# Performance work log

Measured on AMD Instinct MI355X. Metric: run time of the kernel, lower is better.

The kernel has to match this reference:

```python
import jax, jax.numpy as jnp
import numpy as np

B, T, M, D, H, DK, DV = 2, 1024, 1024, 1024, 16, 64, 64
R = 2 * T + M  # number of relative positions required by rel_shift path


def setup_inputs() -> dict:
    key = jax.random.key(0)
    ks = jax.random.split(key, 11)
    s = 0.02
    return {
        "inputs": jax.random.normal(ks[0], (B, T, D), jnp.float32),
        "attention_mask": jnp.ones((B, T, M + T), jnp.float32),
        "positional_encodings": jax.random.normal(ks[1], (R, D), jnp.float32),
        "memory": jax.random.normal(ks[2], (B, M, D), jnp.float32),
        "Wq": jax.random.normal(ks[3], (D, H * DK), jnp.float32) * s,
        "Wk": jax.random.normal(ks[4], (D, H * DK), jnp.float32) * s,
        "Wv": jax.random.normal(ks[5], (D, H * DV), jnp.float32) * s,
        "Wr": jax.random.normal(ks[6], (D, H * DK), jnp.float32) * s,
        "r_w_bias": jax.random.normal(ks[7], (H, DK), jnp.float32) * s,
        "r_r_bias": jax.random.normal(ks[8], (H, DK), jnp.float32) * s,
        "W_out": jax.random.normal(ks[9], (H * DV, D), jnp.float32) * s,
    }


def _rel_shift(m, attention_length):
    # m: [T_q, T_q + L] -> [T_q, L], TXL relative shift via reshape/slice
    tq, total = m.shape
    x = m.reshape(total, tq)[1:].reshape(tq, total - 1)
    return x[:, :attention_length]


def reference(inputs, attention_mask, positional_encodings, memory,
              Wq, Wk, Wv, Wr, r_w_bias, r_r_bias, W_out):
    b, t, d = inputs.shape
    values = jnp.concatenate([memory, inputs], axis=1)  # [B, L, D]
    L = values.shape[1]
    q = (inputs @ Wq).reshape(b, t, H, DK)
    k = (values @ Wk).reshape(b, L, H, DK)
    v = (values @ Wv).reshape(b, L, H, DV)
    rk = (positional_encodings @ Wr).reshape(-1, H, DK)  # [R, H, DK]
    # content + relative logits (TXL)
    content = jnp.einsum('bthd,bThd->bhtT', q + r_w_bias, k)        # [B,H,T,L]
    rel = jnp.einsum('bthd,rhd->bhtr', q + r_r_bias, rk)            # [B,H,T,R]
    rel = jax.vmap(jax.vmap(lambda m: _rel_shift(m, L)))(rel)       # [B,H,T,L]
    logits = (content + rel) * (DK ** -0.5)
    masked = logits - (1.0 - attention_mask[:, None, :, :]) * 1e30
    w = jax.nn.softmax(masked, axis=-1)
    attn = jnp.einsum('bhtT,bThd->bthd', w, v)                      # [B,T,H,DV]
    return attn.reshape(b, t, H * DV) @ W_out
```

## Files before the change

### kernel.cpp

```cpp
#include <hip/hip_runtime.h>
#include <hip/hip_fp16.h>
#include <stdint.h>

#define Bz 2
#define Tq 1024
#define Mm 1024
#define Hh 16
#define Ll 2048
#define Rr 3072

typedef __attribute__((ext_vector_type(8))) short bf16x8;
typedef __attribute__((ext_vector_type(4))) float f32x4;

typedef __attribute__((address_space(3))) uint8_t lds_u8_t;
typedef __attribute__((address_space(1))) uint8_t glb_u8_t;

__device__ __forceinline__ void gl2lds16(const void* g, void* l) {
  __builtin_amdgcn_global_load_lds((const glb_u8_t*)g, (lds_u8_t*)l, 16, 0, 0);
}

__device__ __forceinline__ unsigned short f2bf(float f) {
  unsigned int u = __builtin_bit_cast(unsigned int, f);
  u = u + 0x7fffu + ((u >> 16) & 1u);
  return (unsigned short)(u >> 16);
}
__device__ __forceinline__ float b2f(unsigned short s) {
  unsigned int u = ((unsigned int)s) << 16;
  return __builtin_bit_cast(float, u);
}
__device__ __forceinline__ unsigned int cvt_pk_bf16(float lo, float hi) {
  unsigned int r;
  asm volatile("v_cvt_pk_bf16_f32 %0, %1, %2" : "=v"(r) : "v"(lo), "v"(hi));
  return r;
}

__global__ __launch_bounds__(256) void k_prep2(
    const float* __restrict__ x, const float* __restrict__ mem,
    const float* __restrict__ pos,
    const float* __restrict__ w0, const float* __restrict__ w1,
    const float* __restrict__ w2, const float* __restrict__ w3,
    const float* __restrict__ w4,
    unsigned short* __restrict__ vin, unsigned short* __restrict__ pb,
    unsigned short* __restrict__ t0, unsigned short* __restrict__ t1,
    unsigned short* __restrict__ t2, unsigned short* __restrict__ t3,
    unsigned short* __restrict__ t4) {
  __shared__ float tile[64][65];
  int bid = blockIdx.x;
  if (bid < 4096) {
    int idx = bid * 256 + threadIdx.x;
    int e = idx << 2;
    int row = e >> 10, col = e & 1023;
    int b = row >> 11, l = row & 2047;
    const float* s = (l < Mm) ? (mem + (((size_t)b * Mm + l) << 10) + col)
                              : (x + (((size_t)b * Tq + (l - Mm)) << 10) + col);
    float4 v = *(const float4*)s;
    ushort4 o;
    o.x = f2bf(v.x); o.y = f2bf(v.y); o.z = f2bf(v.z); o.w = f2bf(v.w);
    *(ushort4*)(vin + e) = o;
  } else if (bid < 7168) {
    int idx = (bid - 4096) * 256 + threadIdx.x;
    int e = idx << 2;
    float4 v = *(const float4*)(pos + e);
    ushort4 t;
    t.x = f2bf(v.x); t.y = f2bf(v.y); t.z = f2bf(v.z); t.w = f2bf(v.w);
    *(ushort4*)(pb + e) = t;
  } else {
    int r3 = bid - 7168;
    int mz = r3 >> 8, rem = r3 & 255;
    const float* W;
    unsigned short* WT;
    switch (mz) {
      case 0: W = w0; WT = t0; break;
      case 1: W = w1; WT = t1; break;
      case 2: W = w2; WT = t2; break;
      case 3: W = w3; WT = t3; break;
      default: W = w4; WT = t4; break;
    }
    int k0 = (rem >> 4) * 64, n0 = (rem & 15) * 64;
    int tid = threadIdx.x;
    int rr = tid >> 4, c4 = (tid & 15) * 4;
#pragma unroll
    for (int it = 0; it < 4; ++it) {
      int r = rr + it * 16;
      float4 v = *(const float4*)(W + (size_t)(k0 + r) * 1024 + n0 + c4);
      tile[r][c4] = v.x; tile[r][c4 + 1] = v.y;
      tile[r][c4 + 2] = v.z; tile[r][c4 + 3] = v.w;
    }
    __syncthreads();
#pragma unroll
    for (int it = 0; it < 4; ++it) {
      int n = rr + it * 16;
      ushort4 o;
      o.x = f2bf(tile[c4 + 0][n]); o.y = f2bf(tile[c4 + 1][n]);
      o.z = f2bf(tile[c4 + 2][n]); o.w = f2bf(tile[c4 + 3][n]);
      *(ushort4*)(WT + (size_t)(n0 + n) * 1024 + k0 + c4) = o;
    }
  }
}

template <int RMAP>
__device__ __forceinline__ void gemm_pipe(const unsigned short* __restrict__ A,
                                          const unsigned short* __restrict__ Bt,
                                          int m0, int n0, unsigned short* As,
                                          unsigned short* Bs, f32x4 acc[4][4]) {
  const int tid = threadIdx.x;
  const int w = tid >> 6, lane = tid & 63;
  const int quad = lane >> 4, li = lane & 15;
  const int wr = w >> 1, wc = w & 1;
  f32x4 z = {0.f, 0.f, 0.f, 0.f};
#pragma unroll
  for (int mi = 0; mi < 4; ++mi)
#pragma unroll
    for (int ni = 0; ni < 4; ++ni) acc[mi][ni] = z;

  const int rs = lane >> 2;
  const int cs = lane & 3;

#pragma unroll
  for (int s = 0; s < 2; ++s) {
    int i = w * 2 + s;
    int r = i * 16 + rs;
    int c = cs ^ ((r >> 1) & 3);
    int ar = m0 + r;
    if (RMAP) ar = ar + 1024 + (ar & 1024);
    gl2lds16(A + (size_t)ar * 1024 + c * 8, (char*)As + i * 1024);
    gl2lds16(Bt + (size_t)(n0 + r) * 1024 + c * 8, (char*)Bs + i * 1024);
  }

  for (int k0 = 0; k0 < 1024; k0 += 32) {
    const int bo = ((k0 >> 5) & 1) * 8192;
    const int no = bo ^ 8192;
    __builtin_amdgcn_s_waitcnt(0x0F70);
    __syncthreads();
    if (k0 + 32 < 1024) {
#pragma unroll
      for (int s = 0; s < 2; ++s) {
        int i = w * 2 + s;
        int r = i * 16 + rs;
        int c = cs ^ ((r >> 1) & 3);
        int ar = m0 + r;
        if (RMAP) ar = ar + 1024 + (ar & 1024);
        gl2lds16(A + (size_t)ar * 1024 + k0 + 32 + c * 8,
                 (char*)As + no + i * 1024);
        gl2lds16(Bt + (size_t)(n0 + r) * 1024 + k0 + 32 + c * 8,
                 (char*)Bs + no + i * 1024);
      }
    }
    bf16x8 af[4], bfr[4];
#pragma unroll
    for (int mi = 0; mi < 4; ++mi) {
      int r = wr * 64 + mi * 16 + li;
      int ch = quad ^ ((r >> 1) & 3);
      af[mi] = *(const bf16x8*)((const char*)As + bo + r * 64 + ch * 16);
    }
#pragma unroll
    for (int ni = 0; ni < 4; ++ni) {
      int r = wc * 64 + ni * 16 + li;
      int ch = quad ^ ((r >> 1) & 3);
      bfr[ni] = *(const bf16x8*)((const char*)Bs + bo + r * 64 + ch * 16);
    }
#pragma unroll
    for (int mi = 0; mi < 4; ++mi)
#pragma unroll
      for (int ni = 0; ni < 4; ++ni)
        acc[mi][ni] = __builtin_amdgcn_mfma_f32_16x16x32_bf16(
            af[mi], bfr[ni], acc[mi][ni], 0, 0, 0);
  }
}

__global__ __launch_bounds__(256) void k_proj(
    const unsigned short* __restrict__ Vin, const unsigned short* __restrict__ Pb,
    const unsigned short* __restrict__ WqT, const unsigned short* __restrict__ WkT,
    const unsigned short* __restrict__ WvT, const unsigned short* __restrict__ WrT,
    unsigned short* __restrict__ qb, unsigned short* __restrict__ kb,
    unsigned short* __restrict__ vtb, unsigned short* __restrict__ rkb) {
  __shared__ unsigned short As[2 * 128 * 32];
  __shared__ unsigned short Bs[2 * 128 * 32];
  const int t = blockIdx.x;
  const int tid = threadIdx.x, w = tid >> 6, lane = tid & 63;
  const int quad = lane >> 4, li = lane & 15, wr = w >> 1, wc = w & 1;
  f32x4 acc[4][4];

  if (t < 256) {
    int a = t & 7, n = (t >> 3) & 7, c = t >> 6;
    int m0 = (4 * a + c) * 128, n0 = n * 128;
    gemm_pipe<0>(Vin, WkT, m0, n0, As, Bs, acc);
#pragma unroll
    for (int mi = 0; mi < 4; ++mi)
#pragma unroll
      for (int ni = 0; ni < 4; ++ni)
#pragma unroll
        for (int reg = 0; reg < 4; ++reg) {
          int rrow = m0 + wr * 64 + mi * 16 + quad * 4 + reg;
          int cc = n0 + wc * 64 + ni * 16 + li;
          kb[(size_t)rrow * 1024 + cc] = f2bf(acc[mi][ni][reg]);
        }
  } else if (t < 512) {
    int f = t - 256;
    int a = f & 7, n = (f >> 3) & 7, c = f >> 6;
    int m0 = (4 * a + c) * 128, n0 = n * 128;
    gemm_pipe<0>(Vin, WvT, m0, n0, As, Bs, acc);
#pragma unroll
    for (int mi = 0; mi < 4; ++mi)
#pragma unroll
      for (int ni = 0; ni < 4; ++ni) {
        int r0 = m0 + wr * 64 + mi * 16 + quad * 4;
        int b = r0 >> 11, l0 = r0 & 2047;
        int cc = n0 + wc * 64 + ni * 16 + li;
        ushort4 o;
        o.x = f2bf(acc[mi][ni][0]); o.y = f2bf(acc[mi][ni][1]);
        o.z = f2bf(acc[mi][ni][2]); o.w = f2bf(acc[mi][ni][3]);
        *(ushort4*)(vtb + ((size_t)(b * 1024 + cc)) * Ll + l0) = o;
      }
  } else if (t < 640) {
    int f = t - 512;
    int a = f & 7, n = (f >> 3) & 7, c = f >> 6;
    int m0 = (2 * a + c) * 128, n0 = n * 128;
    gemm_pipe<1>(Vin, WqT, m0, n0, As, Bs, acc);
#pragma unroll
    for (int mi = 0; mi < 4; ++mi)
#pragma unroll
      for (int ni = 0; ni < 4; ++ni)
#pragma unroll
        for (int reg = 0; reg < 4; ++reg) {
          int rrow = m0 + wr * 64 + mi * 16 + quad * 4 + reg;
          int cc = n0 + wc * 64 + ni * 16 + li;
          qb[(size_t)rrow * 1024 + cc] = f2bf(acc[mi][ni][reg]);
        }
  } else {
    int f = t - 640;
    int a = f & 7, n = (f >> 3) & 7, c = f >> 6;
    int m0 = (3 * a + c) * 128, n0 = n * 128;
    gemm_pipe<0>(Pb, WrT, m0, n0, As, Bs, acc);
#pragma unroll
    for (int mi = 0; mi < 4; ++mi)
#pragma unroll
      for (int ni = 0; ni < 4; ++ni)
#pragma unroll
        for (int reg = 0; reg < 4; ++reg) {
          int rrow = m0 + wr * 64 + mi * 16 + quad * 4 + reg;
          int cc = n0 + wc * 64 + ni * 16 + li;
          rkb[(size_t)rrow * 1024 + cc] = f2bf(acc[mi][ni][reg]);
        }
  }
}

__global__ __launch_bounds__(256) void k_gemm_out64(
    const unsigned short* __restrict__ attnb, const unsigned short* __restrict__ WoT,
    float* __restrict__ out) {
  __shared__ unsigned short As[2 * 64 * 32];
  __shared__ unsigned short Bs[2 * 64 * 32];
  int m0 = blockIdx.x * 64, n0 = blockIdx.y * 64;
  const int tid = threadIdx.x, w = tid >> 6, lane = tid & 63;
  const int quad = lane >> 4, li = lane & 15, wr = w >> 1, wc = w & 1;
  f32x4 z = {0.f, 0.f, 0.f, 0.f};
  f32x4 acc[2][2];
#pragma unroll
  for (int mi = 0; mi < 2; ++mi)
#pragma unroll
    for (int ni = 0; ni < 2; ++ni) acc[mi][ni] = z;
  const int rs = lane >> 2, cs = lane & 3;

  {
    int r = w * 16 + rs;
    int c = cs ^ ((r >> 1) & 3);
    gl2lds16(attnb + (size_t)(m0 + r) * 1024 + c * 8, (char*)As + w * 1024);
    gl2lds16(WoT + (size_t)(n0 + r) * 1024 + c * 8, (char*)Bs + w * 1024);
  }

  for (int k0 = 0; k0 < 1024; k0 += 32) {
    const int bo = ((k0 >> 5) & 1) * 4096;
    __builtin_amdgcn_s_waitcnt(0x0F70);
    __syncthreads();
    if (k0 + 32 < 1024) {
      int r = w * 16 + rs;
      int c = cs ^ ((r >> 1) & 3);
      gl2lds16(attnb + (size_t)(m0 + r) * 1024 + k0 + 32 + c * 8,
               (char*)As + (bo ^ 4096) + w * 1024);
      gl2lds16(WoT + (size_t)(n0 + r) * 1024 + k0 + 32 + c * 8,
               (char*)Bs + (bo ^ 4096) + w * 1024);
    }
    bf16x8 af[2], bfr[2];
#pragma unroll
    for (int mi = 0; mi < 2; ++mi) {
      int r = wr * 32 + mi * 16 + li;
      int ch = quad ^ ((r >> 1) & 3);
      af[mi] = *(const bf16x8*)((const char*)As + bo + r * 64 + ch * 16);
    }
#pragma unroll
    for (int ni = 0; ni < 2; ++ni) {
      int r = wc * 32 + ni * 16 + li;
      int ch = quad ^ ((r >> 1) & 3);
      bfr[ni] = *(const bf16x8*)((const char*)Bs + bo + r * 64 + ch * 16);
    }
#pragma unroll
    for (int mi = 0; mi < 2; ++mi)
#pragma unroll
      for (int ni = 0; ni < 2; ++ni)
        acc[mi][ni] = __builtin_amdgcn_mfma_f32_16x16x32_bf16(
            af[mi], bfr[ni], acc[mi][ni], 0, 0, 0);
  }
#pragma unroll
  for (int mi = 0; mi < 2; ++mi)
#pragma unroll
    for (int ni = 0; ni < 2; ++ni)
#pragma unroll
      for (int reg = 0; reg < 4; ++reg) {
        int rrow = m0 + wr * 32 + mi * 16 + quad * 4 + reg;
        int cc = n0 + wc * 32 + ni * 16 + li;
        out[(size_t)rrow * 1024 + cc] = acc[mi][ni][reg];
      }
}

__global__ __launch_bounds__(512, 4) void k_attn(
    const unsigned short* __restrict__ qb, const float* __restrict__ rwb,
    const float* __restrict__ rrb,
    const unsigned short* __restrict__ kb, const unsigned short* __restrict__ vt,
    const unsigned short* __restrict__ rkb, const float* __restrict__ maskf,
    unsigned short* __restrict__ attnb) {
  __shared__ __align__(16) uint8_t lds[75776];

  const int tid = threadIdx.x;
  const int w = tid >> 6, lane = tid & 63;
  const int quad = lane >> 4, li = lane & 15;
  const int wq = w & 3, grp = w >> 2;
  const int srow = lane >> 3, scs = lane & 7;
  const int flat = blockIdx.x + 16 * blockIdx.y + 256 * blockIdx.z;
  const int qt = (flat >> 3) & 15;
  const int g = 4 * (flat & 7) + (flat >> 7);
  const int h = g & 15, b = g >> 4;
  const int t0blk = qt * 64;
  const int t0w = t0blk + wq * 16;
  const int rboff = 48 - 16 * wq;
  const int rbase0 = Tq - t0blk - 63;
  const int jbase = grp * 1024;

  unsigned short* KS = (unsigned short*)(lds + grp * 8192);
  unsigned short* VS = (unsigned short*)(lds + 16384 + grp * 8192);
  unsigned short* RS = (unsigned short*)(lds + 32768 + grp * 16384);
  unsigned short* pw = (unsigned short*)(lds + 65536 + w * 1280);
  float* red = (float*)(lds + 32768);

  const unsigned short* kbase = kb + ((size_t)(b * Ll + jbase) * Hh + h) * 64;
  const unsigned short* vbase = vt + ((size_t)((b * Hh + h) * 64)) * Ll + jbase;
  const unsigned short* rkbase = rkb + (size_t)h * 64;
  const float* mrowf = maskf + ((size_t)(b * Tq + t0w + li)) * Ll + jbase;

  bf16x8 aqw[2], aqr[2];
  {
    const unsigned short* p1 = qb + ((size_t)((b * Tq + t0w + li) * Hh + h)) * 64;
#pragma unroll
    for (int ks = 0; ks < 2; ++ks) {
      bf16x8 qf = *(const bf16x8*)(p1 + ks * 32 + quad * 8);
      const float* wp = rwb + h * 64 + ks * 32 + quad * 8;
      const float* rp = rrb + h * 64 + ks * 32 + quad * 8;
      float4 w0 = *(const float4*)wp, w1 = *(const float4*)(wp + 4);
      float4 r0 = *(const float4*)rp, r1 = *(const float4*)(rp + 4);
      float wv[8] = {w0.x, w0.y, w0.z, w0.w, w1.x, w1.y, w1.z, w1.w};
      float rv[8] = {r0.x, r0.y, r0.z, r0.w, r1.x, r1.y, r1.z, r1.w};
#pragma unroll
      for (int i2 = 0; i2 < 8; ++i2) {
        float qv = b2f((unsigned short)qf[i2]);
        aqw[ks][i2] = (short)f2bf(qv + wv[i2]);
        aqr[ks][i2] = (short)f2bf(qv + rv[i2]);
      }
    }
  }

  f32x4 z = {0.f, 0.f, 0.f, 0.f};
  f32x4 o[4];
  o[0] = z; o[1] = z; o[2] = z; o[3] = z;
  f32x4 ol = z;
  float nmf[8] = {0.f, 0.f, 0.f, 0.f, 0.f, 0.f, 0.f, 0.f};

  const float SC = 0.125f * 1.4426950408889634f;
  const float BIGM = 1.442695e30f;
  const short oneb = 0x3F80;
  const bf16x8 onesf = {oneb, oneb, oneb, oneb, oneb, oneb, oneb, oneb};

  int srcl[4];
#pragma unroll
  for (int reg = 0; reg < 4; ++reg) {
    int row = quad * 4 + reg;
    srcl[reg] = (lane & 48) + ((li + row + 1) & 15);
  }

  auto finish = [&](const unsigned short* VsP, const float (&mv)[8]) {
    bf16x8 sv = *(const bf16x8*)(pw + li * 40 + quad * 8);
    float p[8];
#pragma unroll
    for (int i2 = 0; i2 < 8; ++i2) {
      float sf = __half2float(__builtin_bit_cast(__half, (unsigned short)sv[i2]));
      float mvneg = fmaf(mv[i2], BIGM, -BIGM);
      p[i2] = exp2f(fmaf(sf, SC, mvneg));
    }
    int4 pk;
    pk.x = (int)cvt_pk_bf16(p[0], p[1]);
    pk.y = (int)cvt_pk_bf16(p[2], p[3]);
    pk.z = (int)cvt_pk_bf16(p[4], p[5]);
    pk.w = (int)cvt_pk_bf16(p[6], p[7]);
    bf16x8 apv = __builtin_bit_cast(bf16x8, pk);
    __builtin_amdgcn_s_setprio(1);
    ol = __builtin_amdgcn_mfma_f32_16x16x32_bf16(apv, onesf, ol, 0, 0, 0);
#pragma unroll
    for (int nt = 0; nt < 4; ++nt) {
      int dv = nt * 16 + li;
      int ch = quad ^ ((dv >> 1) & 3);
      bf16x8 vf = *(const bf16x8*)(VsP + dv * 32 + ch * 8);
      o[nt] = __builtin_amdgcn_mfma_f32_16x16x32_bf16(apv, vf, o[nt], 0, 0, 0);
    }
    __builtin_amdgcn_s_setprio(0);
  };

#pragma unroll
  for (int pass = 0; pass < 3; ++pass) {
    int u = pass * 32 + wq * 8 + srow;
    int gr = rbase0 + jbase + u;
    if (gr > Rr - 1) gr = Rr - 1;
    int c = scs ^ srow;
    gl2lds16(rkbase + (size_t)gr * 1024 + c * 8, RS + (pass * 32 + wq * 8) * 64);
  }
  {
    int r = wq * 8 + srow;
    int c = scs ^ srow;
    gl2lds16(kbase + (size_t)r * 1024 + c * 8, KS + wq * 512);
  }

  for (int jt = 0; jt < 32; ++jt) {
    const int jloc = jt * 32;
    __builtin_amdgcn_s_waitcnt(0x0F70);
    __syncthreads();
    if (jt < 31) {
      {
        int r = wq * 8 + srow;
        int c = scs ^ srow;
        gl2lds16(kbase + (size_t)(jloc + 32 + r) * 1024 + c * 8,
                 KS + (((jt + 1) & 1) * 2048) + wq * 512);
      }
      {
        int u = jloc + 96 + wq * 8 + srow;
        int gr = rbase0 + jbase + u;
        if (gr > Rr - 1) gr = Rr - 1;
        int c = scs ^ srow;
        gl2lds16(rkbase + (size_t)gr * 1024 + c * 8,
                 RS + ((jloc + 96 + wq * 8) & 127) * 64);
      }
    }
    {
      int dv = wq * 16 + (lane >> 2);
      int c = (lane & 3) ^ ((dv >> 1) & 3);
      gl2lds16(vbase + (size_t)dv * Ll + jloc + c * 8,
               VS + ((jt & 1) * 2048) + wq * 512);
    }
    asm volatile("" ::: "memory");
    const unsigned short* KsC = KS + (jt & 1) * 2048;
    f32x4 sc[2];
    sc[0] = z; sc[1] = z;
    __builtin_amdgcn_s_setprio(1);
#pragma unroll
    for (int ks = 0; ks < 2; ++ks)
#pragma unroll
      for (int nt = 0; nt < 2; ++nt) {
        int j = nt * 16 + li;
        int ch = (ks * 4 + quad) ^ (j & 7);
        bf16x8 kf = *(const bf16x8*)(KsC + j * 64 + ch * 8);
        sc[nt] = __builtin_amdgcn_mfma_f32_16x16x32_bf16(aqw[ks], kf, sc[nt], 0, 0, 0);
      }
    f32x4 bd[3];
    bd[0] = z; bd[1] = z; bd[2] = z;
#pragma unroll
    for (int ks = 0; ks < 2; ++ks)
#pragma unroll
      for (int nt = 0; nt < 3; ++nt) {
        int pr = (rboff + nt * 16 + li + jloc) & 127;
        int ch = (ks * 4 + quad) ^ (pr & 7);
        bf16x8 rf = *(const bf16x8*)(RS + pr * 64 + ch * 8);
        bd[nt] = __builtin_amdgcn_mfma_f32_16x16x32_bf16(aqr[ks], rf, bd[nt], 0, 0, 0);
      }
    __builtin_amdgcn_s_setprio(0);
    if (jt > 0) finish(VS + ((jt - 1) & 1) * 2048, nmf);
    {
      float4 m0 = *(const float4*)(mrowf + jloc + quad * 8);
      float4 m1 = *(const float4*)(mrowf + jloc + quad * 8 + 4);
      nmf[0] = m0.x; nmf[1] = m0.y; nmf[2] = m0.z; nmf[3] = m0.w;
      nmf[4] = m1.x; nmf[5] = m1.y; nmf[6] = m1.z; nmf[7] = m1.w;
    }
    float rot[2][4];
#pragma unroll
    for (int nt = 0; nt < 2; ++nt)
#pragma unroll
      for (int reg = 0; reg < 4; ++reg)
        rot[nt][reg] = __shfl(sc[nt][reg], srcl[reg], 64);
#pragma unroll
    for (int nt = 0; nt < 3; ++nt)
#pragma unroll
      for (int reg = 0; reg < 4; ++reg) {
        int row = quad * 4 + reg;
        int jj = nt * 16 + li + row - 15;
        int nthi = (nt > 1) ? 0 : nt;
        int ntlo = (nt == 0) ? 0 : (nt - 1);
        float val = ((li + row) >= 15) ? rot[nthi][reg] : rot[ntlo][reg];
        float s = val + bd[nt][reg];
        if ((unsigned)jj < 32u)
          pw[row * 40 + jj] = __builtin_bit_cast(unsigned short, __float2half(s));
      }
  }
  __builtin_amdgcn_s_waitcnt(0x0F70);
  __syncthreads();
  finish(VS + 2048, nmf);

  if (grp == 1) {
    float* rp = red + (size_t)(wq * 64 + lane) * 20;
#pragma unroll
    for (int nt = 0; nt < 4; ++nt)
#pragma unroll
      for (int reg = 0; reg < 4; ++reg) rp[nt * 4 + reg] = o[nt][reg];
#pragma unroll
    for (int reg = 0; reg < 4; ++reg) rp[16 + reg] = ol[reg];
  }
  __syncthreads();
  if (grp == 0) {
    const float* rp = red + (size_t)(wq * 64 + lane) * 20;
    float inv[4];
#pragma unroll
    for (int reg = 0; reg < 4; ++reg) inv[reg] = 1.0f / (ol[reg] + rp[16 + reg]);
#pragma unroll
    for (int nt = 0; nt < 4; ++nt)
#pragma unroll
      for (int reg = 0; reg < 4; ++reg) {
        int trow = t0w + quad * 4 + reg;
        float val = (o[nt][reg] + rp[nt * 4 + reg]) * inv[reg];
        attnb[((size_t)(b * Tq + trow)) * 1024 + h * 64 + nt * 16 + li] = f2bf(val);
      }
  }
}

extern "C" void kernel_launch(void* const* d_in, const int* in_sizes, int n_in,
                              void* d_out, int out_size, void* d_ws, size_t ws_size,
                              hipStream_t stream) {
  const float* x = (const float*)d_in[0];
  const float* mask = (const float*)d_in[1];
  const float* pos = (const float*)d_in[2];
  const float* mem = (const float*)d_in[3];
  const float* Wq = (const float*)d_in[4];
  const float* Wk = (const float*)d_in[5];
  const float* Wv = (const float*)d_in[6];
  const float* Wr = (const float*)d_in[7];
  const float* rwb = (const float*)d_in[8];
  const float* rrb = (const float*)d_in[9];
  const float* Wo = (const float*)d_in[10];
  float* out = (float*)d_out;

  uint8_t* ws = (uint8_t*)d_ws;
  const size_t MB = 1024 * 1024;
  unsigned short* Vinb = (unsigned short*)(ws + 0);
  unsigned short* WqT = (unsigned short*)(ws + 8 * MB);
  unsigned short* WkT = (unsigned short*)(ws + 10 * MB);
  unsigned short* WvT = (unsigned short*)(ws + 12 * MB);
  unsigned short* WrT = (unsigned short*)(ws + 14 * MB);
  unsigned short* WoT = (unsigned short*)(ws + 16 * MB);
  unsigned short* Pb = (unsigned short*)(ws + 18 * MB);
  unsigned short* qb = (unsigned short*)(ws + 24 * MB);
  unsigned short* kb = (unsigned short*)(ws + 32 * MB);
  unsigned short* vtb = (unsigned short*)(ws + 40 * MB);
  unsigned short* rkb = (unsigned short*)(ws + 48 * MB);
  unsigned short* attnb = (unsigned short*)(ws + 19 * MB);

  hipLaunchKernelGGL(k_prep2, dim3(8448), dim3(256), 0, stream,
                     x, mem, pos, Wq, Wk, Wv, Wr, Wo,
                     Vinb, Pb, WqT, WkT, WvT, WrT, WoT);
  hipLaunchKernelGGL(k_proj, dim3(832), dim3(256), 0, stream,
                     Vinb, Pb, WqT, WkT, WvT, WrT, qb, kb, vtb, rkb);
  hipLaunchKernelGGL(k_attn, dim3(16, 16, 2), dim3(512), 0, stream,
                     qb, rwb, rrb, kb, vtb, rkb, mask, attnb);
  hipLaunchKernelGGL(k_gemm_out64, dim3(32, 16), dim3(256), 0, stream,
                     attnb, WoT, out);
}
```

Before: 239.7 us.

## Triple-buffer output projection GEMM with two-stage-ahead async LDS prefetch

Moves the output projection GEMM from double to triple LDS buffering, issuing global-to-LDS loads two k-steps ahead. The wait drops from draining all VM loads to keeping up to two outstanding, and the full __syncthreads becomes a bare s_barrier. This targets load latency that stays exposed with only one stage in flight. In exchange it uses more LDS per block and adds finer-grained waitcnt handling, which risks races if the counts are wrong.

```diff
diff --git a/kernel.cpp b/kernel.cpp
--- a/kernel.cpp
+++ b/kernel.cpp
@@ -248,8 +248,8 @@
 __global__ __launch_bounds__(256) void k_gemm_out64(
     const unsigned short* __restrict__ attnb, const unsigned short* __restrict__ WoT,
     float* __restrict__ out) {
-  __shared__ unsigned short As[2 * 64 * 32];
-  __shared__ unsigned short Bs[2 * 64 * 32];
+  __shared__ unsigned short As[3 * 64 * 32];
+  __shared__ unsigned short Bs[3 * 64 * 32];
   int m0 = blockIdx.x * 64, n0 = blockIdx.y * 64;
   const int tid = threadIdx.x, w = tid >> 6, lane = tid & 63;
   const int quad = lane >> 4, li = lane & 15, wr = w >> 1, wc = w & 1;
@@ -260,38 +260,42 @@
 #pragma unroll
     for (int ni = 0; ni < 2; ++ni) acc[mi][ni] = z;
   const int rs = lane >> 2, cs = lane & 3;
-
-  {
-    int r = w * 16 + rs;
-    int c = cs ^ ((r >> 1) & 3);
-    gl2lds16(attnb + (size_t)(m0 + r) * 1024 + c * 8, (char*)As + w * 1024);
-    gl2lds16(WoT + (size_t)(n0 + r) * 1024 + c * 8, (char*)Bs + w * 1024);
-  }
-
-  for (int k0 = 0; k0 < 1024; k0 += 32) {
-    const int bo = ((k0 >> 5) & 1) * 4096;
-    __builtin_amdgcn_s_waitcnt(0x0F70);
-    __syncthreads();
-    if (k0 + 32 < 1024) {
-      int r = w * 16 + rs;
-      int c = cs ^ ((r >> 1) & 3);
-      gl2lds16(attnb + (size_t)(m0 + r) * 1024 + k0 + 32 + c * 8,
-               (char*)As + (bo ^ 4096) + w * 1024);
-      gl2lds16(WoT + (size_t)(n0 + r) * 1024 + k0 + 32 + c * 8,
-               (char*)Bs + (bo ^ 4096) + w * 1024);
-    }
+  const int r = w * 16 + rs;
+  const int c = cs ^ ((r >> 1) & 3);
+  const unsigned short* aRow = attnb + (size_t)(m0 + r) * 1024 + c * 8;
+  const unsigned short* bRow = WoT + (size_t)(n0 + r) * 1024 + c * 8;
+
+  gl2lds16(aRow, (char*)As + w * 1024);
+  gl2lds16(bRow, (char*)Bs + w * 1024);
+  gl2lds16(aRow + 32, (char*)As + 4096 + w * 1024);
+  gl2lds16(bRow + 32, (char*)Bs + 4096 + w * 1024);
+
+  for (int it = 0; it < 32; ++it) {
+    const int bo = (it % 3) * 4096;
+    if (it < 31)
+      __builtin_amdgcn_s_waitcnt(0x0072);
+    else
+      __builtin_amdgcn_s_waitcnt(0x0070);
+    __builtin_amdgcn_s_barrier();
+    if (it + 2 < 32) {
+      const int nb = ((it + 2) % 3) * 4096;
+      const int k2 = (it + 2) * 32;
+      gl2lds16(aRow + k2, (char*)As + nb + w * 1024);
+      gl2lds16(bRow + k2, (char*)Bs + nb + w * 1024);
+    }
+    asm volatile("" ::: "memory");
     bf16x8 af[2], bfr[2];
 #pragma unroll
     for (int mi = 0; mi < 2; ++mi) {
-      int r = wr * 32 + mi * 16 + li;
-      int ch = quad ^ ((r >> 1) & 3);
-      af[mi] = *(const bf16x8*)((const char*)As + bo + r * 64 + ch * 16);
+      int rr = wr * 32 + mi * 16 + li;
+      int ch = quad ^ ((rr >> 1) & 3);
+      af[mi] = *(const bf16x8*)((const char*)As + bo + rr * 64 + ch * 16);
     }
 #pragma unroll
     for (int ni = 0; ni < 2; ++ni) {
-      int r = wc * 32 + ni * 16 + li;
-      int ch = quad ^ ((r >> 1) & 3);
-      bfr[ni] = *(const bf16x8*)((const char*)Bs + bo + r * 64 + ch * 16);
+      int rr = wc * 32 + ni * 16 + li;
+      int ch = quad ^ ((rr >> 1) & 3);
+      bfr[ni] = *(const bf16x8*)((const char*)Bs + bo + rr * 64 + ch * 16);
     }
 #pragma unroll
     for (int mi = 0; mi < 2; ++mi)
```

New measurement: 235.0 us, median of 2. About the same (-1.9%).
